# Kernel tuning notes

Hardware: AMD Instinct MI355X
Metric: run time of the kernel (lower is better)

## Reference

```python
import math
import jax, jax.numpy as jnp
import numpy as np

B, C, T = 16, 64, 16384
KERNEL_LEN = 128
EPS = 1e-6


def setup_inputs() -> dict:
    key = jax.random.key(0)
    x = jax.random.normal(key, (B, C, T), dtype=jnp.float32)
    # learnable per-channel params at the torch init values
    log_alpha = jnp.full((C,), math.log(0.98 / (1.0 - 0.98)), dtype=jnp.float32)
    log_delta = jnp.full((C,), math.log(2.0), dtype=jnp.float32)
    log_root = jnp.full((C,), math.log(0.5), dtype=jnp.float32)
    log_s = jnp.full((C,), math.log(0.04 / (1.0 - 0.04)), dtype=jnp.float32)
    return {"x": x, "log_alpha": log_alpha, "log_delta": log_delta,
            "log_root": log_root, "log_s": log_s}


def _ema_kernel(log_s, L, dtype):
    # impulse[c, j] = s_c * (1 - s_c)^j, j = lag (0 = most recent)
    s = jax.nn.sigmoid(log_s).astype(dtype)  # (C,)
    j = jnp.arange(KERNEL_LEN, dtype=dtype)  # (Lk,)
    impulse = s[:, None] * (1.0 - s[:, None]) ** j[None, :]  # (C, Lk)
    impulse = impulse / (impulse.sum(axis=1, keepdims=True) + 1e-8)
    kernel = impulse[:, ::-1]              # causal conv: flip in time
    kernel = kernel[:, -L:]                # truncate if T < Lk
    return kernel[:, None, :]              # (C, 1, L) -> OIH for depthwise


def reference(x, log_alpha, log_delta, log_root, log_s):
    _, Cc, Tt = x.shape
    L = min(KERNEL_LEN, Tt)
    alpha = jax.nn.sigmoid(log_alpha)              # (C,)
    delta = jax.nn.softplus(log_delta) + 1e-6      # (C,)
    root = jax.nn.softplus(log_root) + 0.1         # (C,)

    x_mag = jnp.abs(x)                             # (B, C, T)
    kernel = _ema_kernel(log_s, L, x.dtype)        # (C, 1, L)
    x_pad = jnp.pad(x_mag, ((0, 0), (0, 0), (L - 1, 0)))  # causal left-pad
    M = jax.lax.conv_general_dilated(
        x_pad, kernel,
        window_strides=(1,), padding='VALID',
        dimension_numbers=('NCH', 'OIH', 'NCH'),
        feature_group_count=Cc)                     # (B, C, T) depthwise EMA

    alpha_bc = alpha[None, :, None]
    delta_bc = delta[None, :, None]
    root_bc = root[None, :, None]
    gain = (EPS + M) ** alpha_bc
    normed = x_mag / gain
    pcen = (normed + delta_bc) ** root_bc - delta_bc ** root_bc
    return pcen
```

## Files before the change

### kernel.cpp

```cpp
#include <hip/hip_runtime.h>
#include <math.h>

namespace {

constexpr int kT = 16384;
constexpr int kC = 64;
constexpr int kL = 128;
constexpr int kThreads = 256;
constexpr int kChunk = 8;
constexpr int kTile = kThreads * kChunk;
constexpr int kHaloChunks = kL / kChunk;
constexpr float kEps = 1e-6f;

__device__ __forceinline__ float fexp2(float v) { return __builtin_amdgcn_exp2f(v); }
__device__ __forceinline__ float flog2(float v) { return __builtin_amdgcn_logf(v); }

constexpr float kLog2e  = 1.4426950408889634f;
constexpr float kRlog2e = 0.6931471805599453f;

__device__ __forceinline__ float fsigmoid(float z) {
  return 1.f / (1.f + fexp2(-z * kLog2e));
}
__device__ __forceinline__ float fsoftplus(float v) {
  return flog2(1.f + fexp2(v * kLog2e)) * kRlog2e;
}

__device__ __forceinline__ float4 ld4g(const float* p) { return *(const float4*)p; }

__global__ __launch_bounds__(kThreads) void pcen_kernel(
    const float* __restrict__ x,
    const float* __restrict__ log_alpha,
    const float* __restrict__ log_delta,
    const float* __restrict__ log_root,
    const float* __restrict__ log_s,
    float* __restrict__ out)
{
  __shared__ float bsum[kHaloChunks + kThreads];

  const int tid = threadIdx.x;
  const int row = blockIdx.x >> 3;
  const int tb  = (blockIdx.x & 7) * kTile;
  const int c   = row & (kC - 1);

  const float* __restrict__ xr   = x + (size_t)row * kT;
  float* __restrict__       outr = out + (size_t)row * kT;

  const int base = tb + kChunk * tid;

  const float4 v0 = ld4g(xr + base);
  const float4 v1 = ld4g(xr + base + 4);
  float4 o0 = make_float4(0.f, 0.f, 0.f, 0.f);
  float4 o1 = o0;
  if (base >= kL) {
    o0 = ld4g(xr + base - kL);
    o1 = ld4g(xr + base - kL + 4);
  }
  float4 h0 = make_float4(0.f, 0.f, 0.f, 0.f);
  float4 h1 = h0;
  if (tid < kHaloChunks && tb) {
    h0 = ld4g(xr + tb - kL + kChunk * tid);
    h1 = ld4g(xr + tb - kL + kChunk * tid + 4);
  }

  const float s    = fsigmoid(log_s[c]);
  const float r    = 1.f - s;
  const float r2   = r * r;
  const float r4   = r2 * r2;
  const float r8   = r4 * r4;
  const float r16  = r8 * r8;
  const float r32  = r16 * r16;
  const float r64  = r32 * r32;
  const float r128 = r64 * r64;
  const float kn   = s / ((1.f - r128) + 1e-8f);
  const float alpha = fsigmoid(log_alpha[c]);
  const float delta = fsoftplus(log_delta[c]) + 1e-6f;
  const float root  = fsoftplus(log_root[c]) + 0.1f;
  const float dr    = fexp2(root * flog2(delta));

  float Bv = fabsf(v0.x);
  Bv = fmaf(Bv, r, fabsf(v0.y)); Bv = fmaf(Bv, r, fabsf(v0.z));
  Bv = fmaf(Bv, r, fabsf(v0.w)); Bv = fmaf(Bv, r, fabsf(v1.x));
  Bv = fmaf(Bv, r, fabsf(v1.y)); Bv = fmaf(Bv, r, fabsf(v1.z));
  Bv = fmaf(Bv, r, fabsf(v1.w));
  bsum[kHaloChunks + tid] = Bv;
  if (tid < kHaloChunks) {
    float Bh = fabsf(h0.x);
    Bh = fmaf(Bh, r, fabsf(h0.y)); Bh = fmaf(Bh, r, fabsf(h0.z));
    Bh = fmaf(Bh, r, fabsf(h0.w)); Bh = fmaf(Bh, r, fabsf(h1.x));
    Bh = fmaf(Bh, r, fabsf(h1.y)); Bh = fmaf(Bh, r, fabsf(h1.z));
    Bh = fmaf(Bh, r, fabsf(h1.w));
    bsum[tid] = Bh;
  }
  __syncthreads();

  float Sa = bsum[tid + 0];
  float Sb = bsum[tid + 1];
  #pragma unroll
  for (int i = 2; i < kHaloChunks; i += 2) {
    Sa = fmaf(Sa, r16, bsum[tid + i]);
    Sb = fmaf(Sb, r16, bsum[tid + i + 1]);
  }
  float S = fmaf(Sa, r8, Sb);

  const float xv[kChunk] = {fabsf(v0.x), fabsf(v0.y), fabsf(v0.z), fabsf(v0.w),
                            fabsf(v1.x), fabsf(v1.y), fabsf(v1.z), fabsf(v1.w)};
  const float ol[kChunk] = {fabsf(o0.x), fabsf(o0.y), fabsf(o0.z), fabsf(o0.w),
                            fabsf(o1.x), fabsf(o1.y), fabsf(o1.z), fabsf(o1.w)};
  float res[kChunk];
  #pragma unroll
  for (int j = 0; j < kChunk; ++j) {
    S = fmaf(S, r, xv[j]);
    S = fmaf(-r128, ol[j], S);
    const float M      = kn * S;
    const float ginv   = fexp2(-alpha * flog2(kEps + M));
    const float normed = xv[j] * ginv;
    res[j] = fexp2(root * flog2(normed + delta)) - dr;
  }

  *(float4*)(outr + base)     = make_float4(res[0], res[1], res[2], res[3]);
  *(float4*)(outr + base + 4) = make_float4(res[4], res[5], res[6], res[7]);
}

}

extern "C" void kernel_launch(void* const* d_in, const int* in_sizes, int n_in,
                              void* d_out, int out_size, void* d_ws, size_t ws_size,
                              hipStream_t stream) {
  const float* x  = (const float*)d_in[0];
  const float* la = (const float*)d_in[1];
  const float* ld = (const float*)d_in[2];
  const float* lr = (const float*)d_in[3];
  const float* ls = (const float*)d_in[4];
  float* out = (float*)d_out;

  constexpr int rows = 16 * 64;
  constexpr int blocksPerRow = kT / kTile;
  constexpr int grid = rows * blocksPerRow;

  hipLaunchKernelGGL(pcen_kernel, dim3(grid), dim3(kThreads), 0, stream,
                     x, la, ld, lr, ls, out);
}
```

Before: 26.76 us.

## Process four sub-tiles per block with halo reuse and next-tile prefetch

```diff
diff --git a/kernel.cpp b/kernel.cpp
--- a/kernel.cpp
+++ b/kernel.cpp
@@ -8,8 +8,10 @@
 constexpr int kL = 128;
 constexpr int kThreads = 256;
 constexpr int kChunk = 8;
-constexpr int kTile = kThreads * kChunk;
-constexpr int kHaloChunks = kL / kChunk;
+constexpr int kSub = kThreads * kChunk;
+constexpr int kSpan = 8192;
+constexpr int kIters = kSpan / kSub;
+constexpr int kHC = kL / kChunk;
 constexpr float kEps = 1e-6f;
 
 __device__ __forceinline__ float fexp2(float v) { return __builtin_amdgcn_exp2f(v); }
@@ -27,7 +29,16 @@
 
 __device__ __forceinline__ float4 ld4g(const float* p) { return *(const float4*)p; }
 
-__global__ __launch_bounds__(kThreads) void pcen_kernel(
+__device__ __forceinline__ float horner8(float4 a, float4 b, float r) {
+  float B = fabsf(a.x);
+  B = fmaf(B, r, fabsf(a.y)); B = fmaf(B, r, fabsf(a.z));
+  B = fmaf(B, r, fabsf(a.w)); B = fmaf(B, r, fabsf(b.x));
+  B = fmaf(B, r, fabsf(b.y)); B = fmaf(B, r, fabsf(b.z));
+  B = fmaf(B, r, fabsf(b.w));
+  return B;
+}
+
+__global__ __launch_bounds__(kThreads, 8) void pcen_kernel(
     const float* __restrict__ x,
     const float* __restrict__ log_alpha,
     const float* __restrict__ log_delta,
@@ -35,31 +46,28 @@
     const float* __restrict__ log_s,
     float* __restrict__ out)
 {
-  __shared__ float bsum[kHaloChunks + kThreads];
+  __shared__ float bs[2][kHC + kThreads];
 
   const int tid = threadIdx.x;
-  const int row = blockIdx.x >> 3;
-  const int tb  = (blockIdx.x & 7) * kTile;
+  const int row = blockIdx.x >> 1;
+  const int tb0 = (blockIdx.x & 1) * kSpan;
   const int c   = row & (kC - 1);
 
   const float* __restrict__ xr   = x + (size_t)row * kT;
   float* __restrict__       outr = out + (size_t)row * kT;
 
-  const int base = tb + kChunk * tid;
-
-  const float4 v0 = ld4g(xr + base);
-  const float4 v1 = ld4g(xr + base + 4);
-  float4 o0 = make_float4(0.f, 0.f, 0.f, 0.f);
-  float4 o1 = o0;
-  if (base >= kL) {
-    o0 = ld4g(xr + base - kL);
-    o1 = ld4g(xr + base - kL + 4);
+  const int base0 = tb0 + kChunk * tid;
+  float4 v0 = ld4g(xr + base0);
+  float4 v1 = ld4g(xr + base0 + 4);
+  float4 o0 = make_float4(0.f, 0.f, 0.f, 0.f), o1 = o0;
+  if (base0 >= kL) {
+    o0 = ld4g(xr + base0 - kL);
+    o1 = ld4g(xr + base0 - kL + 4);
   }
-  float4 h0 = make_float4(0.f, 0.f, 0.f, 0.f);
-  float4 h1 = h0;
-  if (tid < kHaloChunks && tb) {
-    h0 = ld4g(xr + tb - kL + kChunk * tid);
-    h1 = ld4g(xr + tb - kL + kChunk * tid + 4);
+  float4 h0 = make_float4(0.f, 0.f, 0.f, 0.f), h1 = h0;
+  if (tid < kHC && tb0) {
+    h0 = ld4g(xr + tb0 - kL + kChunk * tid);
+    h1 = ld4g(xr + tb0 - kL + kChunk * tid + 4);
   }
 
   const float s    = fsigmoid(log_s[c]);
@@ -77,48 +85,55 @@
   const float root  = fsoftplus(log_root[c]) + 0.1f;
   const float dr    = fexp2(root * flog2(delta));
 
-  float Bv = fabsf(v0.x);
-  Bv = fmaf(Bv, r, fabsf(v0.y)); Bv = fmaf(Bv, r, fabsf(v0.z));
-  Bv = fmaf(Bv, r, fabsf(v0.w)); Bv = fmaf(Bv, r, fabsf(v1.x));
-  Bv = fmaf(Bv, r, fabsf(v1.y)); Bv = fmaf(Bv, r, fabsf(v1.z));
-  Bv = fmaf(Bv, r, fabsf(v1.w));
-  bsum[kHaloChunks + tid] = Bv;
-  if (tid < kHaloChunks) {
-    float Bh = fabsf(h0.x);
-    Bh = fmaf(Bh, r, fabsf(h0.y)); Bh = fmaf(Bh, r, fabsf(h0.z));
-    Bh = fmaf(Bh, r, fabsf(h0.w)); Bh = fmaf(Bh, r, fabsf(h1.x));
-    Bh = fmaf(Bh, r, fabsf(h1.y)); Bh = fmaf(Bh, r, fabsf(h1.z));
-    Bh = fmaf(Bh, r, fabsf(h1.w));
-    bsum[tid] = Bh;
+  if (tid < kHC) bs[0][tid] = horner8(h0, h1, r);
+
+  #pragma unroll
+  for (int i = 0; i < kIters; ++i) {
+    const int b  = i & 1;
+    const int cb = tb0 + i * kSub + kChunk * tid;
+
+    float4 nv0, nv1, no0, no1;
+    if (i < kIters - 1) {
+      nv0 = ld4g(xr + cb + kSub);
+      nv1 = ld4g(xr + cb + kSub + 4);
+      no0 = ld4g(xr + cb + kSub - kL);
+      no1 = ld4g(xr + cb + kSub - kL + 4);
+    }
+
+    bs[b][kHC + tid] = horner8(v0, v1, r);
+    if (i > 0 && tid < kHC)
+      bs[b][tid] = bs[1 - b][kThreads + tid];
+    __syncthreads();
+
+    float Sa = bs[b][tid + 0];
+    float Sb = bs[b][tid + 1];
+    #pragma unroll
+    for (int m = 2; m < kHC; m += 2) {
+      Sa = fmaf(Sa, r16, bs[b][tid + m]);
+      Sb = fmaf(Sb, r16, bs[b][tid + m + 1]);
+    }
+    float S = fmaf(Sa, r8, Sb);
+
+    const float xv[kChunk] = {fabsf(v0.x), fabsf(v0.y), fabsf(v0.z), fabsf(v0.w),
+                              fabsf(v1.x), fabsf(v1.y), fabsf(v1.z), fabsf(v1.w)};
+    const float ol[kChunk] = {fabsf(o0.x), fabsf(o0.y), fabsf(o0.z), fabsf(o0.w),
+                              fabsf(o1.x), fabsf(o1.y), fabsf(o1.z), fabsf(o1.w)};
+    float res[kChunk];
+    #pragma unroll
+    for (int j = 0; j < kChunk; ++j) {
+      S = fmaf(S, r, xv[j]);
+      S = fmaf(-r128, ol[j], S);
+      const float M      = kn * S;
+      const float ginv   = fexp2(-alpha * flog2(kEps + M));
+      const float normed = xv[j] * ginv;
+      res[j] = fexp2(root * flog2(normed + delta)) - dr;
+    }
+
+    *(float4*)(outr + cb)     = make_float4(res[0], res[1], res[2], res[3]);
+    *(float4*)(outr + cb + 4) = make_float4(res[4], res[5], res[6], res[7]);
+
+    if (i < kIters - 1) { v0 = nv0; v1 = nv1; o0 = no0; o1 = no1; }
   }
-  __syncthreads();
-
-  float Sa = bsum[tid + 0];
-  float Sb = bsum[tid + 1];
-  #pragma unroll
-  for (int i = 2; i < kHaloChunks; i += 2) {
-    Sa = fmaf(Sa, r16, bsum[tid + i]);
-    Sb = fmaf(Sb, r16, bsum[tid + i + 1]);
-  }
-  float S = fmaf(Sa, r8, Sb);
-
-  const float xv[kChunk] = {fabsf(v0.x), fabsf(v0.y), fabsf(v0.z), fabsf(v0.w),
-                            fabsf(v1.x), fabsf(v1.y), fabsf(v1.z), fabsf(v1.w)};
-  const float ol[kChunk] = {fabsf(o0.x), fabsf(o0.y), fabsf(o0.z), fabsf(o0.w),
-                            fabsf(o1.x), fabsf(o1.y), fabsf(o1.z), fabsf(o1.w)};
-  float res[kChunk];
-  #pragma unroll
-  for (int j = 0; j < kChunk; ++j) {
-    S = fmaf(S, r, xv[j]);
-    S = fmaf(-r128, ol[j], S);
-    const float M      = kn * S;
-    const float ginv   = fexp2(-alpha * flog2(kEps + M));
-    const float normed = xv[j] * ginv;
-    res[j] = fexp2(root * flog2(normed + delta)) - dr;
-  }
-
-  *(float4*)(outr + base)     = make_float4(res[0], res[1], res[2], res[3]);
-  *(float4*)(outr + base + 4) = make_float4(res[4], res[5], res[6], res[7]);
 }
 
 }
@@ -134,7 +149,7 @@
   float* out = (float*)d_out;
 
   constexpr int rows = 16 * 64;
-  constexpr int blocksPerRow = kT / kTile;
+  constexpr int blocksPerRow = kT / kSpan;
   constexpr int grid = rows * blocksPerRow;
 
   hipLaunchKernelGGL(pcen_kernel, dim3(grid), dim3(kThreads), 0, stream,
```

Result: faster. 25.77 us (median of 2 runs) (-3.7%).
